# Performance work log

Hardware: AMD Instinct MI355X
Metric: run time of the kernel (lower is better)

## Reference

```python
import jax, jax.numpy as jnp
import numpy as np

ALPHA_F, GAMMA_F = 0.25, 2.0   # focal loss params
SMOOTH = 1e-6                  # dice smooth
THETA = 5.0                    # boundary weight
W_FOCAL, W_DICE, W_BOUND = 0.3, 0.4, 0.3


def _erode(m):
    # one iteration of scipy binary_erosion, cross (connectivity-1) structure,
    # border_value=0 (outside treated as False)
    p = jnp.pad(m, ((0, 0), (0, 0), (1, 1), (1, 1)), constant_values=False)
    c = p[:, :, 1:-1, 1:-1]
    up = p[:, :, :-2, 1:-1]
    dn = p[:, :, 2:, 1:-1]
    lf = p[:, :, 1:-1, :-2]
    rt = p[:, :, 1:-1, 2:]
    return c & up & dn & lf & rt


def _dilate(m):
    # one iteration of scipy binary_dilation, cross structure, border_value=0
    p = jnp.pad(m, ((0, 0), (0, 0), (1, 1), (1, 1)), constant_values=False)
    c = p[:, :, 1:-1, 1:-1]
    up = p[:, :, :-2, 1:-1]
    dn = p[:, :, 2:, 1:-1]
    lf = p[:, :, 1:-1, :-2]
    rt = p[:, :, 1:-1, 2:]
    return c | up | dn | lf | rt


def setup_inputs() -> dict:
    key = jax.random.key(0)
    k1, k2 = jax.random.split(key)
    B, C, H, W = 64, 1, 512, 512
    inputs = jax.random.normal(k1, (B, C, H, W), dtype=jnp.float32)
    targets = jax.random.randint(k2, (B, C, H, W), 0, 2).astype(jnp.float32)
    return {"inputs": inputs, "targets": targets}


def reference(inputs, targets):
    # numerically stable BCE-with-logits, elementwise
    bce = jnp.maximum(inputs, 0.0) - inputs * targets + jnp.log1p(jnp.exp(-jnp.abs(inputs)))

    # --- focal loss ---
    pt = jnp.exp(-bce)
    focal_loss = jnp.mean(ALPHA_F * (1.0 - pt) ** GAMMA_F * bce)

    # --- dice loss ---
    p = jax.nn.sigmoid(inputs)
    intersection = jnp.sum(p * targets)
    dice = (2.0 * intersection + SMOOTH) / (jnp.sum(p) + jnp.sum(targets) + SMOOTH)
    dice_loss = 1.0 - dice

    # --- boundary-weighted BCE ---
    mask = targets > 0.5
    eroded = _erode(_erode(mask))      # iterations=2
    dilated = _dilate(_dilate(mask))   # iterations=2
    boundary = dilated & (~eroded)
    weights = boundary.astype(jnp.float32) * THETA + 1.0
    boundary_loss = jnp.mean(bce * weights)

    return W_FOCAL * focal_loss + W_DICE * dice_loss + W_BOUND * boundary_loss
```

## Files before the change

### kernel.cpp

```cpp
#include <hip/hip_runtime.h>
#include <math.h>

static constexpr int Hdim = 512;
static constexpr int Wdim = 512;
static constexpr int HW   = Hdim * Wdim;
static constexpr int NIMG = 64;
static constexpr int WPR  = Wdim / 64;
static constexpr int TOTAL_WORDS = NIMG * Hdim * WPR;
static constexpr int RSTRIP = 32;
static constexpr int SPI  = Hdim / RSTRIP;
static constexpr int NBLK = NIMG * SPI;
static constexpr int MROWS = RSTRIP + 4;
static constexpr int NBLK_A = 2048;
static constexpr int NIT = (RSTRIP * Wdim) / (256 * 4);


__global__ __launch_bounds__(256) void mask_kernel(
    const float* __restrict__ tgt, unsigned long long* __restrict__ mask)
{
    const int lane = threadIdx.x & 63;
    const int wid  = (blockIdx.x * 256 + threadIdx.x) >> 6;
    #pragma unroll
    for (int g = 0; g < 8; g++) {
        int w0 = wid * 32 + g * 4;
        float v0 = tgt[(w0 + 0) * 64 + lane];
        float v1 = tgt[(w0 + 1) * 64 + lane];
        float v2 = tgt[(w0 + 2) * 64 + lane];
        float v3 = tgt[(w0 + 3) * 64 + lane];
        unsigned long long m0 = __ballot(v0 > 0.5f);
        unsigned long long m1 = __ballot(v1 > 0.5f);
        unsigned long long m2 = __ballot(v2 > 0.5f);
        unsigned long long m3 = __ballot(v3 > 0.5f);
        if (lane == 0) {
            mask[w0 + 0] = m0;
            mask[w0 + 1] = m1;
            mask[w0 + 2] = m2;
            mask[w0 + 3] = m3;
        }
    }
}

__device__ __forceinline__ unsigned long long shl1(unsigned long long c, unsigned long long l) {
    return (c << 1) | (l >> 63);
}
__device__ __forceinline__ unsigned long long shr1(unsigned long long c, unsigned long long r) {
    return (c >> 1) | (r << 63);
}
__device__ __forceinline__ unsigned long long shl2(unsigned long long c, unsigned long long l) {
    return (c << 2) | (l >> 62);
}
__device__ __forceinline__ unsigned long long shr2(unsigned long long c, unsigned long long r) {
    return (c >> 2) | (r << 62);
}

__global__ __launch_bounds__(256) void combined_loss_kernel(
    const float* __restrict__ inp, const unsigned long long* __restrict__ mask,
    float* __restrict__ partials)
{
    __shared__ unsigned long long tmask[MROWS][WPR];
    __shared__ unsigned long long bmask[RSTRIP][WPR];
    __shared__ float smem[4][5];

    const int img   = blockIdx.x / SPI;
    const int strip = blockIdx.x % SPI;
    const int r0    = strip * RSTRIP;
    const float* ib = inp + img * HW;
    const unsigned long long* mb = mask + img * Hdim * WPR;

    const int wave = threadIdx.x >> 6;
    const int lane = threadIdx.x & 63;

    #pragma unroll
    for (int c = threadIdx.x; c < MROWS * WPR; c += 256) {
        int row  = c >> 3;
        int word = c & 7;
        int gr   = r0 - 2 + row;
        unsigned long long v = 0ULL;
        if ((unsigned)gr < (unsigned)Hdim) v = mb[gr * WPR + word];
        tmask[row][word] = v;
    }
    __syncthreads();

    {
        int row  = threadIdx.x >> 3;
        int word = threadIdx.x & 7;
        int mr = row + 2;

        #define CW(r)  tmask[r][word]
        #define LW(r)  (word > 0 ? tmask[r][word - 1] : 0ULL)
        #define RW(r)  (word < WPR - 1 ? tmask[r][word + 1] : 0ULL)
        unsigned long long c0 = CW(mr),   l0 = LW(mr),   rr0 = RW(mr);
        unsigned long long cm = CW(mr-1), lm = LW(mr-1), rm  = RW(mr-1);
        unsigned long long cp = CW(mr+1), lp = LW(mr+1), rp  = RW(mr+1);
        unsigned long long cm2 = CW(mr-2);
        unsigned long long cp2 = CW(mr+2);
        #undef CW
        #undef LW
        #undef RW

        unsigned long long er =
            c0 & shl1(c0,l0) & shr1(c0,rr0) & shl2(c0,l0) & shr2(c0,rr0)
               & cm & shl1(cm,lm) & shr1(cm,rm)
               & cp & shl1(cp,lp) & shr1(cp,rp)
               & cm2 & cp2;
        unsigned long long di =
            c0 | shl1(c0,l0) | shr1(c0,rr0) | shl2(c0,l0) | shr2(c0,rr0)
               | cm | shl1(cm,lm) | shr1(cm,rm)
               | cp | shl1(cp,lp) | shr1(cp,rp)
               | cm2 | cp2;
        bmask[row][word] = di & ~er;
    }
    __syncthreads();

    float s_focal = 0.f, s_inter = 0.f, s_p = 0.f, s_bw = 0.f;
    int s_tc = 0;

    const float* base = ib + r0 * Wdim + threadIdx.x * 4;
    float4 cur = *(const float4*)(base);
    #pragma unroll
    for (int it = 0; it < NIT; it++) {
        float4 nxt;
        if (it + 1 < NIT) nxt = *(const float4*)(base + (it + 1) * 1024);

        int flat = it * 1024 + threadIdx.x * 4;
        int row  = flat >> 9;
        int x    = flat & (Wdim - 1);
        unsigned int tb4 = (unsigned int)((tmask[row + 2][x >> 6] >> (x & 63)) & 0xFULL);
        unsigned int bb4 = (unsigned int)((bmask[row][x >> 6]     >> (x & 63)) & 0xFULL);
        s_tc += __popc(tb4);
        const float xs[4] = {cur.x, cur.y, cur.z, cur.w};
        #pragma unroll
        for (int k = 0; k < 4; k++) {
            float xi = xs[k];
            bool tpos = (tb4 >> k) & 1;
            float e  = __expf(-fabsf(xi));
            float bce = fmaxf(xi, 0.f) - (tpos ? xi : 0.f) + __logf(1.f + e);
            float rden = __builtin_amdgcn_rcpf(1.f + e);
            float p = (xi >= 0.f ? 1.f : e) * rden;
            float pt = tpos ? p : 1.f - p;
            float om = 1.f - pt;
            s_focal += 0.25f * om * om * bce;
            s_p     += p;
            s_inter += tpos ? p : 0.f;
            float wgt = ((bb4 >> k) & 1) ? 6.0f : 1.0f;
            s_bw += bce * wgt;
        }
        cur = nxt;
    }
    float s_t = (float)s_tc;

    #pragma unroll
    for (int off = 32; off > 0; off >>= 1) {
        s_focal += __shfl_down(s_focal, off);
        s_inter += __shfl_down(s_inter, off);
        s_p     += __shfl_down(s_p,     off);
        s_t     += __shfl_down(s_t,     off);
        s_bw    += __shfl_down(s_bw,    off);
    }
    if (lane == 0) {
        smem[wave][0] = s_focal; smem[wave][1] = s_inter; smem[wave][2] = s_p;
        smem[wave][3] = s_t;     smem[wave][4] = s_bw;
    }
    __syncthreads();
    if (threadIdx.x < 5) {
        float a = smem[0][threadIdx.x] + smem[1][threadIdx.x]
                + smem[2][threadIdx.x] + smem[3][threadIdx.x];
        partials[blockIdx.x * 8 + threadIdx.x] = a;
    }
}

__global__ __launch_bounds__(256) void finalize_kernel(
    const float* __restrict__ partials, float* __restrict__ out)
{
    __shared__ float smem[4][5];
    float a0 = 0.f, a1 = 0.f, a2 = 0.f, a3 = 0.f, a4 = 0.f;
    for (int b = threadIdx.x; b < NBLK; b += 256) {
        const float* s = partials + b * 8;
        a0 += s[0]; a1 += s[1]; a2 += s[2]; a3 += s[3]; a4 += s[4];
    }
    #pragma unroll
    for (int off = 32; off > 0; off >>= 1) {
        a0 += __shfl_down(a0, off);
        a1 += __shfl_down(a1, off);
        a2 += __shfl_down(a2, off);
        a3 += __shfl_down(a3, off);
        a4 += __shfl_down(a4, off);
    }
    int wave = threadIdx.x >> 6;
    int lane = threadIdx.x & 63;
    if (lane == 0) {
        smem[wave][0] = a0; smem[wave][1] = a1; smem[wave][2] = a2;
        smem[wave][3] = a3; smem[wave][4] = a4;
    }
    __syncthreads();
    if (threadIdx.x == 0) {
        double b0 = 0, b1 = 0, b2 = 0, b3 = 0, b4 = 0;
        #pragma unroll
        for (int w = 0; w < 4; w++) {
            b0 += smem[w][0]; b1 += smem[w][1]; b2 += smem[w][2];
            b3 += smem[w][3]; b4 += smem[w][4];
        }
        double invN = 1.0 / (double)(NIMG * HW);
        double focal_loss = b0 * invN;
        double dice = (2.0 * b1 + 1e-6) / (b2 + b3 + 1e-6);
        double boundary_loss = b4 * invN;
        out[0] = (float)(0.3 * focal_loss + 0.4 * (1.0 - dice) + 0.3 * boundary_loss);
    }
}

extern "C" void kernel_launch(void* const* d_in, const int* in_sizes, int n_in,
                              void* d_out, int out_size, void* d_ws, size_t ws_size,
                              hipStream_t stream) {
    const float* inp = (const float*)d_in[0];
    const float* tgt = (const float*)d_in[1];
    float* out = (float*)d_out;
    float* partials = (float*)d_ws;
    unsigned long long* mask = (unsigned long long*)((char*)d_ws + 65536);

    mask_kernel<<<NBLK_A, 256, 0, stream>>>(tgt, mask);
    combined_loss_kernel<<<NBLK, 256, 0, stream>>>(inp, mask, partials);
    finalize_kernel<<<1, 256, 0, stream>>>(partials, out);
}
```

Measured before the change: 151.5 us.

## Fuse target bitmask construction into the loss kernel, dropping mask pre-pass

Removes the separate mask kernel and has each strip block read its 36 halo rows of targets directly, ballot them into bitmasks and store them in shared memory. This avoids one kernel launch and the global write and read of the packed mask. In exchange, halo rows are read twice by neighboring blocks (about 12% extra target traffic), and each block now does four dependent ballot groups before it can start the main loss loop.

```diff
diff --git a/kernel.cpp b/kernel.cpp
--- a/kernel.cpp
+++ b/kernel.cpp
@@ -6,78 +6,70 @@
 static constexpr int HW   = Hdim * Wdim;
 static constexpr int NIMG = 64;
 static constexpr int WPR  = Wdim / 64;
-static constexpr int TOTAL_WORDS = NIMG * Hdim * WPR;
 static constexpr int RSTRIP = 32;
 static constexpr int SPI  = Hdim / RSTRIP;
 static constexpr int NBLK = NIMG * SPI;
 static constexpr int MROWS = RSTRIP + 4;
-static constexpr int NBLK_A = 2048;
 static constexpr int NIT = (RSTRIP * Wdim) / (256 * 4);
-
-
-__global__ __launch_bounds__(256) void mask_kernel(
-    const float* __restrict__ tgt, unsigned long long* __restrict__ mask)
+static constexpr int WORDS_PER_WAVE = (MROWS * WPR) / 4;
+
+
+__device__ __forceinline__ unsigned long long shl1(unsigned long long c, unsigned long long l) {
+    return (c << 1) | (l >> 63);
+}
+__device__ __forceinline__ unsigned long long shr1(unsigned long long c, unsigned long long r) {
+    return (c >> 1) | (r << 63);
+}
+__device__ __forceinline__ unsigned long long shl2(unsigned long long c, unsigned long long l) {
+    return (c << 2) | (l >> 62);
+}
+__device__ __forceinline__ unsigned long long shr2(unsigned long long c, unsigned long long r) {
+    return (c >> 2) | (r << 62);
+}
+
+__global__ __launch_bounds__(256) void combined_loss_kernel(
+    const float* __restrict__ inp, const float* __restrict__ tgt,
+    float* __restrict__ partials)
 {
+    __shared__ unsigned long long tmask[MROWS][WPR];
+    __shared__ unsigned long long bmask[RSTRIP][WPR];
+    __shared__ float smem[4][5];
+
+    const int img   = blockIdx.x / SPI;
+    const int strip = blockIdx.x % SPI;
+    const int r0    = strip * RSTRIP;
+    const float* ib = inp + img * HW;
+    const float* tb = tgt + img * HW;
+
+    const int wave = threadIdx.x >> 6;
     const int lane = threadIdx.x & 63;
-    const int wid  = (blockIdx.x * 256 + threadIdx.x) >> 6;
-    #pragma unroll
-    for (int g = 0; g < 8; g++) {
-        int w0 = wid * 32 + g * 4;
-        float v0 = tgt[(w0 + 0) * 64 + lane];
-        float v1 = tgt[(w0 + 1) * 64 + lane];
-        float v2 = tgt[(w0 + 2) * 64 + lane];
-        float v3 = tgt[(w0 + 3) * 64 + lane];
+
+    unsigned long long* tmflat = &tmask[0][0];
+    const int wi_base = wave * WORDS_PER_WAVE;
+    #pragma unroll
+    for (int g = 0; g < WORDS_PER_WAVE / 4; g++) {
+        int wi0 = wi_base + g * 4;
+        float v0 = 0.f, v1 = 0.f, v2 = 0.f, v3 = 0.f;
+        {
+            int gr0 = r0 - 2 + ((wi0 + 0) >> 3);
+            int gr1 = r0 - 2 + ((wi0 + 1) >> 3);
+            int gr2 = r0 - 2 + ((wi0 + 2) >> 3);
+            int gr3 = r0 - 2 + ((wi0 + 3) >> 3);
+            if ((unsigned)gr0 < (unsigned)Hdim) v0 = tb[gr0 * Wdim + ((wi0 + 0) & 7) * 64 + lane];
+            if ((unsigned)gr1 < (unsigned)Hdim) v1 = tb[gr1 * Wdim + ((wi0 + 1) & 7) * 64 + lane];
+            if ((unsigned)gr2 < (unsigned)Hdim) v2 = tb[gr2 * Wdim + ((wi0 + 2) & 7) * 64 + lane];
+            if ((unsigned)gr3 < (unsigned)Hdim) v3 = tb[gr3 * Wdim + ((wi0 + 3) & 7) * 64 + lane];
+        }
         unsigned long long m0 = __ballot(v0 > 0.5f);
         unsigned long long m1 = __ballot(v1 > 0.5f);
         unsigned long long m2 = __ballot(v2 > 0.5f);
         unsigned long long m3 = __ballot(v3 > 0.5f);
         if (lane == 0) {
-            mask[w0 + 0] = m0;
-            mask[w0 + 1] = m1;
-            mask[w0 + 2] = m2;
-            mask[w0 + 3] = m3;
-        }
-    }
-}
-
-__device__ __forceinline__ unsigned long long shl1(unsigned long long c, unsigned long long l) {
-    return (c << 1) | (l >> 63);
-}
-__device__ __forceinline__ unsigned long long shr1(unsigned long long c, unsigned long long r) {
-    return (c >> 1) | (r << 63);
-}
-__device__ __forceinline__ unsigned long long shl2(unsigned long long c, unsigned long long l) {
-    return (c << 2) | (l >> 62);
-}
-__device__ __forceinline__ unsigned long long shr2(unsigned long long c, unsigned long long r) {
-    return (c >> 2) | (r << 62);
-}
-
-__global__ __launch_bounds__(256) void combined_loss_kernel(
-    const float* __restrict__ inp, const unsigned long long* __restrict__ mask,
-    float* __restrict__ partials)
-{
-    __shared__ unsigned long long tmask[MROWS][WPR];
-    __shared__ unsigned long long bmask[RSTRIP][WPR];
-    __shared__ float smem[4][5];
-
-    const int img   = blockIdx.x / SPI;
-    const int strip = blockIdx.x % SPI;
-    const int r0    = strip * RSTRIP;
-    const float* ib = inp + img * HW;
-    const unsigned long long* mb = mask + img * Hdim * WPR;
-
-    const int wave = threadIdx.x >> 6;
-    const int lane = threadIdx.x & 63;
-
-    #pragma unroll
-    for (int c = threadIdx.x; c < MROWS * WPR; c += 256) {
-        int row  = c >> 3;
-        int word = c & 7;
-        int gr   = r0 - 2 + row;
-        unsigned long long v = 0ULL;
-        if ((unsigned)gr < (unsigned)Hdim) v = mb[gr * WPR + word];
-        tmask[row][word] = v;
+            tmflat[wi0 + 0] = m0;
+            tmflat[wi0 + 1] = m1;
+            tmflat[wi0 + 2] = m2;
+            tmflat[wi0 + 3] = m3;
+        }
     }
     __syncthreads();
 
@@ -215,9 +207,7 @@
     const float* tgt = (const float*)d_in[1];
     float* out = (float*)d_out;
     float* partials = (float*)d_ws;
-    unsigned long long* mask = (unsigned long long*)((char*)d_ws + 65536);
-
-    mask_kernel<<<NBLK_A, 256, 0, stream>>>(tgt, mask);
-    combined_loss_kernel<<<NBLK, 256, 0, stream>>>(inp, mask, partials);
+
+    combined_loss_kernel<<<NBLK, 256, 0, stream>>>(inp, tgt, partials);
     finalize_kernel<<<1, 256, 0, stream>>>(partials, out);
 }
```

Result: slower. 174.8 us (+15.4%).

## Split boundary mask into separate kernel and use grid-stride coalesced loss loop

Applied to the files above, without the earlier changes.

Moves the erosion/dilation boundary computation out of the loss kernel into its own kernel, which writes interleaved target/boundary bit words to global memory. The loss kernel no longer uses shared-memory staging or barriers. It runs a fixed 2048-block grid-stride loop over the flat float4 input and reads the packed mask pairs per float4. This removes the per-block halo loads and syncs, at the cost of an extra launch and a small extra global mask round trip.

```diff
diff --git a/kernel.cpp b/kernel.cpp
--- a/kernel.cpp
+++ b/kernel.cpp
@@ -6,13 +6,14 @@
 static constexpr int HW   = Hdim * Wdim;
 static constexpr int NIMG = 64;
 static constexpr int WPR  = Wdim / 64;
-static constexpr int TOTAL_WORDS = NIMG * Hdim * WPR;
-static constexpr int RSTRIP = 32;
-static constexpr int SPI  = Hdim / RSTRIP;
-static constexpr int NBLK = NIMG * SPI;
-static constexpr int MROWS = RSTRIP + 4;
+static constexpr int WPI  = Hdim * WPR;
+static constexpr int TOTAL_WORDS = NIMG * WPI;
 static constexpr int NBLK_A = 2048;
-static constexpr int NIT = (RSTRIP * Wdim) / (256 * 4);
+static constexpr int NBLK_B = TOTAL_WORDS / 256;
+static constexpr int NBLK_C = 2048;
+static constexpr int CTHREADS = NBLK_C * 256;
+static constexpr int F4TOTAL = NIMG * HW / 4;
+static constexpr int CITERS = F4TOTAL / CTHREADS;
 
 
 __global__ __launch_bounds__(256) void mask_kernel(
@@ -53,82 +54,64 @@
     return (c >> 2) | (r << 62);
 }
 
-__global__ __launch_bounds__(256) void combined_loss_kernel(
-    const float* __restrict__ inp, const unsigned long long* __restrict__ mask,
+__global__ __launch_bounds__(256) void boundary_kernel(
+    const unsigned long long* __restrict__ mask, unsigned long long* __restrict__ comb)
+{
+    const int w = blockIdx.x * 256 + threadIdx.x;
+    const int word = w & 7;
+    const int row  = (w >> 3) & (Hdim - 1);
+    const unsigned long long* mi = mask + (w & ~(WPI - 1));
+
+    #define FW(r, c) ((((unsigned)(r)) < (unsigned)Hdim && ((unsigned)(c)) < (unsigned)WPR) \
+                        ? mi[((r) << 3) + (c)] : 0ULL)
+    unsigned long long c0  = FW(row,     word);
+    unsigned long long l0  = FW(row,     word - 1);
+    unsigned long long rr0 = FW(row,     word + 1);
+    unsigned long long cm  = FW(row - 1, word);
+    unsigned long long lm  = FW(row - 1, word - 1);
+    unsigned long long rm  = FW(row - 1, word + 1);
+    unsigned long long cp  = FW(row + 1, word);
+    unsigned long long lp  = FW(row + 1, word - 1);
+    unsigned long long rp  = FW(row + 1, word + 1);
+    unsigned long long cm2 = FW(row - 2, word);
+    unsigned long long cp2 = FW(row + 2, word);
+    #undef FW
+
+    unsigned long long er =
+        c0 & shl1(c0,l0) & shr1(c0,rr0) & shl2(c0,l0) & shr2(c0,rr0)
+           & cm & shl1(cm,lm) & shr1(cm,rm)
+           & cp & shl1(cp,lp) & shr1(cp,rp)
+           & cm2 & cp2;
+    unsigned long long di =
+        c0 | shl1(c0,l0) | shr1(c0,rr0) | shl2(c0,l0) | shr2(c0,rr0)
+           | cm | shl1(cm,lm) | shr1(cm,rm)
+           | cp | shl1(cp,lp) | shr1(cp,rp)
+           | cm2 | cp2;
+
+    comb[2 * w]     = c0;
+    comb[2 * w + 1] = di & ~er;
+}
+
+__global__ __launch_bounds__(256, 4) void combined_loss_kernel(
+    const float* __restrict__ inp, const unsigned long long* __restrict__ comb,
     float* __restrict__ partials)
 {
-    __shared__ unsigned long long tmask[MROWS][WPR];
-    __shared__ unsigned long long bmask[RSTRIP][WPR];
-    __shared__ float smem[4][5];
-
-    const int img   = blockIdx.x / SPI;
-    const int strip = blockIdx.x % SPI;
-    const int r0    = strip * RSTRIP;
-    const float* ib = inp + img * HW;
-    const unsigned long long* mb = mask + img * Hdim * WPR;
-
-    const int wave = threadIdx.x >> 6;
-    const int lane = threadIdx.x & 63;
-
-    #pragma unroll
-    for (int c = threadIdx.x; c < MROWS * WPR; c += 256) {
-        int row  = c >> 3;
-        int word = c & 7;
-        int gr   = r0 - 2 + row;
-        unsigned long long v = 0ULL;
-        if ((unsigned)gr < (unsigned)Hdim) v = mb[gr * WPR + word];
-        tmask[row][word] = v;
-    }
-    __syncthreads();
-
-    {
-        int row  = threadIdx.x >> 3;
-        int word = threadIdx.x & 7;
-        int mr = row + 2;
-
-        #define CW(r)  tmask[r][word]
-        #define LW(r)  (word > 0 ? tmask[r][word - 1] : 0ULL)
-        #define RW(r)  (word < WPR - 1 ? tmask[r][word + 1] : 0ULL)
-        unsigned long long c0 = CW(mr),   l0 = LW(mr),   rr0 = RW(mr);
-        unsigned long long cm = CW(mr-1), lm = LW(mr-1), rm  = RW(mr-1);
-        unsigned long long cp = CW(mr+1), lp = LW(mr+1), rp  = RW(mr+1);
-        unsigned long long cm2 = CW(mr-2);
-        unsigned long long cp2 = CW(mr+2);
-        #undef CW
-        #undef LW
-        #undef RW
-
-        unsigned long long er =
-            c0 & shl1(c0,l0) & shr1(c0,rr0) & shl2(c0,l0) & shr2(c0,rr0)
-               & cm & shl1(cm,lm) & shr1(cm,rm)
-               & cp & shl1(cp,lp) & shr1(cp,rp)
-               & cm2 & cp2;
-        unsigned long long di =
-            c0 | shl1(c0,l0) | shr1(c0,rr0) | shl2(c0,l0) | shr2(c0,rr0)
-               | cm | shl1(cm,lm) | shr1(cm,rm)
-               | cp | shl1(cp,lp) | shr1(cp,rp)
-               | cm2 | cp2;
-        bmask[row][word] = di & ~er;
-    }
-    __syncthreads();
-
+    const int tid = blockIdx.x * 256 + threadIdx.x;
     float s_focal = 0.f, s_inter = 0.f, s_p = 0.f, s_bw = 0.f;
     int s_tc = 0;
 
-    const float* base = ib + r0 * Wdim + threadIdx.x * 4;
-    float4 cur = *(const float4*)(base);
-    #pragma unroll
-    for (int it = 0; it < NIT; it++) {
-        float4 nxt;
-        if (it + 1 < NIT) nxt = *(const float4*)(base + (it + 1) * 1024);
-
-        int flat = it * 1024 + threadIdx.x * 4;
-        int row  = flat >> 9;
-        int x    = flat & (Wdim - 1);
-        unsigned int tb4 = (unsigned int)((tmask[row + 2][x >> 6] >> (x & 63)) & 0xFULL);
-        unsigned int bb4 = (unsigned int)((bmask[row][x >> 6]     >> (x & 63)) & 0xFULL);
+    #pragma unroll
+    for (int it = 0; it < CITERS; it++) {
+        const int f4 = tid + it * CTHREADS;
+        const float4 v = ((const float4*)inp)[f4];
+        const int wi = f4 >> 4;
+        const int sh = (f4 & 15) * 4;
+        const unsigned long long tw = comb[2 * wi];
+        const unsigned long long bw = comb[2 * wi + 1];
+        unsigned int tb4 = (unsigned int)((tw >> sh) & 0xFULL);
+        unsigned int bb4 = (unsigned int)((bw >> sh) & 0xFULL);
         s_tc += __popc(tb4);
-        const float xs[4] = {cur.x, cur.y, cur.z, cur.w};
+        const float xs[4] = {v.x, v.y, v.z, v.w};
         #pragma unroll
         for (int k = 0; k < 4; k++) {
             float xi = xs[k];
@@ -145,10 +128,12 @@
             float wgt = ((bb4 >> k) & 1) ? 6.0f : 1.0f;
             s_bw += bce * wgt;
         }
-        cur = nxt;
     }
     float s_t = (float)s_tc;
 
+    __shared__ float smem[4][5];
+    const int wave = threadIdx.x >> 6;
+    const int lane = threadIdx.x & 63;
     #pragma unroll
     for (int off = 32; off > 0; off >>= 1) {
         s_focal += __shfl_down(s_focal, off);
@@ -174,7 +159,7 @@
 {
     __shared__ float smem[4][5];
     float a0 = 0.f, a1 = 0.f, a2 = 0.f, a3 = 0.f, a4 = 0.f;
-    for (int b = threadIdx.x; b < NBLK; b += 256) {
+    for (int b = threadIdx.x; b < NBLK_C; b += 256) {
         const float* s = partials + b * 8;
         a0 += s[0]; a1 += s[1]; a2 += s[2]; a3 += s[3]; a4 += s[4];
     }
@@ -214,10 +199,13 @@
     const float* inp = (const float*)d_in[0];
     const float* tgt = (const float*)d_in[1];
     float* out = (float*)d_out;
-    float* partials = (float*)d_ws;
-    unsigned long long* mask = (unsigned long long*)((char*)d_ws + 65536);
-
-    mask_kernel<<<NBLK_A, 256, 0, stream>>>(tgt, mask);
-    combined_loss_kernel<<<NBLK, 256, 0, stream>>>(inp, mask, partials);
+    char* ws = (char*)d_ws;
+    float* partials = (float*)ws;
+    unsigned long long* tmask = (unsigned long long*)(ws + (1u << 20));
+    unsigned long long* comb  = (unsigned long long*)(ws + (4u << 20));
+
+    mask_kernel<<<NBLK_A, 256, 0, stream>>>(tgt, tmask);
+    boundary_kernel<<<NBLK_B, 256, 0, stream>>>(tmask, comb);
+    combined_loss_kernel<<<NBLK_C, 256, 0, stream>>>(inp, comb, partials);
     finalize_kernel<<<1, 256, 0, stream>>>(partials, out);
 }
```

Measured after the change: 152.3 us. About the same (+0.5%).
